# Kernel optimization log

Measured on AMD Instinct MI355X. Metric: run time of the kernel, lower is better.

Reference implementation:

```python
import jax, jax.numpy as jnp
import numpy as np
from jax import lax

N_TAGS = 512
N_TOKENS = 50257
SEQ_LEN = 8192


def setup_inputs() -> dict:
    key = jax.random.key(0)
    k1, k2, k3, k4 = jax.random.split(key, 4)
    token_list = jax.random.randint(k1, (SEQ_LEN,), 0, N_TOKENS, dtype=jnp.int64 if jax.config.read('jax_enable_x64') else jnp.int32)
    # Row-stochastic A [N,N], B [N,M]; Pi [N] sums to 1 (as produced by fit()).
    a = jax.random.uniform(k2, (N_TAGS, N_TAGS), dtype=jnp.float32) + 1e-3
    A = a / a.sum(axis=1, keepdims=True)
    b = jax.random.uniform(k3, (N_TAGS, N_TOKENS), dtype=jnp.float32) + 1e-3
    B = b / b.sum(axis=1, keepdims=True)
    p = jax.random.uniform(k4, (N_TAGS,), dtype=jnp.float32) + 1e-3
    Pi = p / p.sum()
    return {"token_list": token_list, "A": A, "B": B, "Pi": Pi}


def _viterbi(token_list, A, B, Pi):
    N = A.shape[0]
    logA = jnp.log(A)          # [N, N] transition (i -> j)
    logB = jnp.log(B)          # [N, M] emission
    logPi = jnp.log(Pi)        # [N]
    avg_score = jnp.log(jnp.ones((N,), dtype=A.dtype) / N)

    # Emission log-probs per step: [T, N]. token_id == -1 -> uniform score.
    emis = jnp.where((token_list == -1)[:, None], avg_score[None, :], logB.T[token_list])

    v0 = logPi + emis[0]       # [N]

    def step(v, e_t):
        scores = v[:, None] + logA           # [N_prev, N_cur]
        bp = jnp.argmax(scores, axis=0).astype(jnp.int32)   # [N]
        v_new = jnp.max(scores, axis=0) + e_t                # [N]
        return v_new, bp

    v_last, back_pointers = lax.scan(step, v0, emis[1:])  # back_pointers: [T-1, N]

    last = jnp.argmax(v_last).astype(jnp.int32)

    def back(ptr, bp_t):
        prev = bp_t[ptr]
        return prev, prev

    _, path_rev = lax.scan(back, last, back_pointers[::-1])  # [T-1] states T-2..0
    path = jnp.concatenate([path_rev[::-1], last[None]])      # [T] best path, start->end
    return path, v_last


def reference(token_list, A, B, Pi):
    path, _ = _viterbi(token_list, A, B, Pi)
    return path
```

## Files before the change

kernel.cpp:

```cpp
#include <hip/hip_runtime.h>
#include <cstdint>
#include <cstddef>
#include <math.h>


#define NT 512
#define TT 8192
#define MT 50257
#define DELTA_W 0.15f
#define NEG_INF (-3.402823466e38f)

#define BT_L 32
#define BT_S (TT / BT_L)

#define WS_LOGPI   0u
#define WS_VLAST   2048u
#define WS_BOUND   4096u
#define WS_ROWMAX  5632u
#define WS_MAPS    8192u
#define WS_LA      270336u
#define WS_EMIS    1318912u
#define WS_BP      18096128u
#define WS_NEED    26484736u

__global__ void prep_logs(const float* __restrict__ A, const float* __restrict__ Pi,
                          float* __restrict__ lA, float* __restrict__ logPi) {
    int idx = blockIdx.x * blockDim.x + threadIdx.x;
    if (idx < NT * NT) {
        lA[idx] = (float)log((double)A[idx]);
    } else if (idx < NT * NT + NT) {
        int j = idx - NT * NT;
        logPi[j] = (float)log((double)Pi[j]);
    }
}

__global__ void prep_rowmax(const float* __restrict__ lA, float* __restrict__ rowmax) {
    __shared__ float s[4];
    int i = blockIdx.x;
    int t = threadIdx.x;
    float m = fmaxf(lA[i * NT + t], lA[i * NT + t + 256]);
    for (int k = 32; k >= 1; k >>= 1) m = fmaxf(m, __shfl_xor(m, k, 64));
    if ((t & 63) == 0) s[t >> 6] = m;
    __syncthreads();
    if (t == 0) {
        float r = fmaxf(fmaxf(s[0], s[1]), fmaxf(s[2], s[3]));
        rowmax[i] = r;
    }
}

__global__ void prep_emis(const float* __restrict__ B, const int* __restrict__ tok,
                          float* __restrict__ emis) {
    int idx = blockIdx.x * blockDim.x + threadIdx.x;
    if (idx >= TT * NT) return;
    int t = idx >> 9;
    int j = idx & (NT - 1);
    int tk = tok[t];
    float e;
    if (tk < 0) e = (float)log((double)(1.0f / 512.0f));
    else        e = (float)log((double)B[(size_t)j * MT + tk]);
    emis[idx] = e;
}

__launch_bounds__(NT, 1)
__global__ void viterbi_fwd_exact(const float* __restrict__ lA,
                                  const float* __restrict__ rowmax,
                                  const float* emis,
                                  const float* __restrict__ logPi,
                                  unsigned short* __restrict__ bp,
                                  float* __restrict__ vlast,
                                  float* scratch) {
    __shared__ float2 SV[2][560];
    __shared__ float2 SVX[560];
    __shared__ alignas(16) float redR[8];
    __shared__ alignas(16) float redT[8];
    __shared__ int nCtr[2];
    __shared__ int nCtrX;
    __shared__ int Pshare;
    __shared__ float2 part[8][NT];

    const int tid  = threadIdx.x;
    const int j    = tid;
    const int lane = tid & 63;
    const int wave = tid >> 6;
    const unsigned long long below = (1ull << lane) - 1ull;
    const float* __restrict__ lAj = lA + j;

    float acc = 0.0f;
    {
        const float4* lAf4 = (const float4*)lA;
        for (int k = tid; k < (NT * NT) / 4; k += NT) acc += lAf4[k].x;
    }
    float r = rowmax[j];
    const float rmaxOwn = r;
    #pragma unroll
    for (int d = 1; d <= 32; d <<= 1) r = fmaxf(r, __shfl_xor(r, d, 64));
    if (lane == 0) redR[wave] = r;
    if (tid == 0) { nCtr[0] = 0; nCtr[1] = 0; nCtrX = 0; }
    __syncthreads();
    if (acc == 1.2345e30f && j == 511) SVX[0].x = acc;

    float v = logPi[j] + emis[j];
    float e_next = __builtin_nontemporal_load(emis + (size_t)NT + j);
    long long c0 = 0;
    int xSteps = 0;
    if (tid == 0) c0 = clock64();

    for (int t = 1; t < TT; ++t) {
        const int p = t & 1;
        const float e = e_next;
        {
            const int tn = (t + 1 < TT) ? t + 1 : TT - 1;
            e_next = __builtin_nontemporal_load(emis + (size_t)tn * NT + j);
        }
        float wm = v;
        #pragma unroll
        for (int d = 1; d <= 32; d <<= 1) wm = fmaxf(wm, __shfl_xor(wm, d, 64));
        bool pred = (v >= wm - DELTA_W);
        unsigned long long mk = __ballot(pred);
        int base = 0;
        if (lane == 0) base = atomicAdd(&nCtr[p], __popcll(mk));
        base = __shfl(base, 0, 64);
        if (pred) SV[p][base + __popcll(mk & below)] = make_float2(v, __int_as_float(j));
        __syncthreads();

        const int n   = nCtr[p];
        const int nm1 = n - 1;
        if (tid == 0) { nCtr[p ^ 1] = 0; nCtrX = 0; }

        float mv[8]; int bi[8];
        #pragma unroll
        for (int k = 0; k < 8; ++k) { mv[k] = NEG_INF; bi[k] = 0x7fffffff; }
        {
            const float* lAl = lA + lane;
            float ga[4][8], va[4]; int ia[4];
            float gb[4][8], vb[4]; int ib[4];
            #pragma unroll
            for (int q = 0; q < 4; ++q) {
                int s = wave + (q << 3); int gs = s < n ? s : nm1;
                float2 sv = SV[p][gs]; va[q] = sv.x; ia[q] = __float_as_int(sv.y);
                const float* rp = lAl + ((size_t)(unsigned)ia[q] << 9);
                #pragma unroll
                for (int k = 0; k < 8; ++k) ga[q][k] = rp[k << 6];
            }
            int s0 = wave;
            while (true) {
                const int sB = s0 + 32;
                const bool moreB = (sB < n);
                if (moreB) {
                    #pragma unroll
                    for (int q = 0; q < 4; ++q) {
                        int s = sB + (q << 3); int gs = s < n ? s : nm1;
                        float2 sv = SV[p][gs]; vb[q] = sv.x; ib[q] = __float_as_int(sv.y);
                        const float* rp = lAl + ((size_t)(unsigned)ib[q] << 9);
                        #pragma unroll
                        for (int k = 0; k < 8; ++k) gb[q][k] = rp[k << 6];
                    }
                }
                #pragma unroll
                for (int q = 0; q < 4; ++q)
                    #pragma unroll
                    for (int k = 0; k < 8; ++k) {
                        float sc = va[q] + ga[q][k];
                        if (sc > mv[k] || (sc == mv[k] && ia[q] < bi[k])) {
                            mv[k] = sc; bi[k] = ia[q];
                        }
                    }
                if (!moreB) break;
                const int sA = sB + 32;
                const bool moreA = (sA < n);
                if (moreA) {
                    #pragma unroll
                    for (int q = 0; q < 4; ++q) {
                        int s = sA + (q << 3); int gs = s < n ? s : nm1;
                        float2 sv = SV[p][gs]; va[q] = sv.x; ia[q] = __float_as_int(sv.y);
                        const float* rp = lAl + ((size_t)(unsigned)ia[q] << 9);
                        #pragma unroll
                        for (int k = 0; k < 8; ++k) ga[q][k] = rp[k << 6];
                    }
                }
                #pragma unroll
                for (int q = 0; q < 4; ++q)
                    #pragma unroll
                    for (int k = 0; k < 8; ++k) {
                        float sc = vb[q] + gb[q][k];
                        if (sc > mv[k] || (sc == mv[k] && ib[q] < bi[k])) {
                            mv[k] = sc; bi[k] = ib[q];
                        }
                    }
                if (!moreA) break;
                s0 = sA;
            }
        }
        #pragma unroll
        for (int k = 0; k < 8; ++k)
            part[wave][lane + (k << 6)] = make_float2(mv[k], __int_as_float(bi[k]));
        __syncthreads();

        float mval = NEG_INF;
        int   bidx = 0x7fffffff;
        #pragma unroll
        for (int w = 0; w < 8; ++w) {
            const float2 q = part[w][j];
            const float val = q.x;
            const int   ii  = __float_as_int(q.y);
            if (val > mval || (val == mval && ii < bidx)) { mval = val; bidx = ii; }
        }
        float tmin = mval;
        #pragma unroll
        for (int d = 1; d <= 32; d <<= 1) tmin = fminf(tmin, __shfl_xor(tmin, d, 64));
        if (lane == 0) redT[wave] = tmin;
        __syncthreads();

        float4 t0 = *(const float4*)redT;
        float4 t1 = *(const float4*)(redT + 4);
        float T = fminf(fminf(fminf(t0.x, t0.y), fminf(t0.z, t0.w)),
                        fminf(fminf(t1.x, t1.y), fminf(t1.z, t1.w)));
        bool px = (v + rmaxOwn >= T) && !pred;
        unsigned long long mkx = __ballot(px);
        if (mkx != 0ull) {
            int bx = 0;
            if (lane == 0) bx = atomicAdd(&nCtrX, __popcll(mkx));
            bx = __shfl(bx, 0, 64);
            if (px) SVX[bx + __popcll(mkx & below)] = make_float2(v, __int_as_float(j));
        }
        __syncthreads();

        const int nX = nCtrX;
        if (nX > 0) {
            ++xSteps;
            for (int s0x = 0; s0x < nX; s0x += 16) {
                float2 q[16];
                #pragma unroll
                for (int k = 0; k < 16; ++k) {
                    int s = s0x + k;
                    q[k] = SVX[s < nX ? s : nX - 1];
                }
                float a[16];
                #pragma unroll
                for (int k = 0; k < 16; ++k)
                    a[k] = lAj[(size_t)__float_as_int(q[k].y) * NT];
                #pragma unroll
                for (int k = 0; k < 16; ++k) {
                    float sc = q[k].x + a[k];
                    int   is = __float_as_int(q[k].y);
                    if (sc > mval || (sc == mval && is < bidx)) { mval = sc; bidx = is; }
                }
            }
        }
        float vn = mval + e;
        __builtin_nontemporal_store((unsigned short)bidx, bp + (size_t)t * NT + j);
        if (t == TT - 1) vlast[j] = vn;
        v = vn;
    }

    if (tid == 0) {
        long long cyc = (clock64() - c0) / (long long)(TT - 1);
        int cb = (int)(cyc >> 8); if (cb > 255) cb = 255; if (cb < 0) cb = 0;
        int xb = 0; { unsigned x = (unsigned)xSteps; while (x) { ++xb; x >>= 1; } }
        if (xb > 15) xb = 15;
        Pshare = cb * 16 + xb;
    }
    __syncthreads();
    const int P = Pshare;
    for (int pg = 0; pg < P; ++pg) {
        unsigned long long val = ((unsigned long long)pg << 32) | (unsigned)tid;
        __builtin_nontemporal_store(val,
            (unsigned long long*)((char*)scratch + (size_t)pg * 4096) + tid);
    }
}

__launch_bounds__(NT, 1)
__global__ void bt_maps(const unsigned short* __restrict__ bp,
                        unsigned short* __restrict__ maps) {
    __shared__ unsigned short bps[BT_L * NT];
    const int s = blockIdx.x;
    const int tlo = BT_L * s + 1;
    int thi = BT_L * (s + 1); if (thi > TT - 1) thi = TT - 1;
    const int nt = thi - tlo + 1;
    for (int k = threadIdx.x; k < nt * NT; k += NT)
        bps[k] = bp[(size_t)tlo * NT + k];
    __syncthreads();
    int cur = threadIdx.x;
    for (int r = nt - 1; r >= 0; --r) cur = bps[r * NT + cur];
    maps[s * NT + threadIdx.x] = (unsigned short)cur;
}

__launch_bounds__(NT, 1)
__global__ void bt_bound(const float* __restrict__ vlast,
                         const unsigned short* __restrict__ maps,
                         int* __restrict__ bound) {
    __shared__ float sv[NT];
    __shared__ int   si[NT];
    int j = threadIdx.x;
    sv[j] = vlast[j]; si[j] = j;
    __syncthreads();
    for (int off = NT / 2; off > 0; off >>= 1) {
        if (j < off) {
            float v2 = sv[j + off]; int i2 = si[j + off];
            if (v2 > sv[j] || (v2 == sv[j] && i2 < si[j])) { sv[j] = v2; si[j] = i2; }
        }
        __syncthreads();
    }
    if (j == 0) {
        int cur = si[0];
        bound[BT_S] = cur;
        for (int s = BT_S - 1; s >= 0; --s) {
            cur = maps[s * NT + cur];
            bound[s] = cur;
        }
    }
}

__launch_bounds__(NT, 1)
__global__ void bt_path(const unsigned short* __restrict__ bp,
                        const int* __restrict__ bound,
                        int* __restrict__ path) {
    __shared__ unsigned short bps[BT_L * NT];
    const int s = blockIdx.x;
    const int tlo = BT_L * s + 1;
    int thi = BT_L * (s + 1); if (thi > TT - 1) thi = TT - 1;
    const int nt = thi - tlo + 1;
    for (int k = threadIdx.x; k < nt * NT; k += NT)
        bps[k] = bp[(size_t)tlo * NT + k];
    __syncthreads();
    if (threadIdx.x == 0) {
        int cur = bound[s + 1];
        if (s == BT_S - 1) path[TT - 1] = cur;
        for (int r = nt - 1; r >= 0; --r) {
            cur = bps[r * NT + cur];
            path[tlo - 1 + r] = cur;
        }
    }
}

extern "C" void kernel_launch(void* const* d_in, const int* in_sizes, int n_in,
                              void* d_out, int out_size, void* d_ws, size_t ws_size,
                              hipStream_t stream) {
    const int*   tok = (const int*)d_in[0];
    const float* A   = (const float*)d_in[1];
    const float* B   = (const float*)d_in[2];
    const float* Pi  = (const float*)d_in[3];
    int* path = (int*)d_out;
    char* ws = (char*)d_ws;
    if (ws_size < (size_t)WS_NEED) return;

    float* logPi          = (float*)(ws + WS_LOGPI);
    float* vlast          = (float*)(ws + WS_VLAST);
    int*   bound          = (int*)(ws + WS_BOUND);
    float* rowmax         = (float*)(ws + WS_ROWMAX);
    unsigned short* maps  = (unsigned short*)(ws + WS_MAPS);
    float* lA             = (float*)(ws + WS_LA);
    float* emis           = (float*)(ws + WS_EMIS);
    unsigned short* bpp   = (unsigned short*)(ws + WS_BP);

    prep_logs  <<<(NT * NT + NT + 255) / 256, 256, 0, stream>>>(A, Pi, lA, logPi);
    prep_emis  <<<(TT * NT) / 256,            256, 0, stream>>>(B, tok, emis);
    prep_rowmax<<<NT, 256, 0, stream>>>(lA, rowmax);
    viterbi_fwd_exact<<<1, NT, 0, stream>>>(lA, rowmax, emis, logPi, bpp, vlast,
                                            emis );
    bt_maps  <<<BT_S, NT, 0, stream>>>(bpp, maps);
    bt_bound <<<1,    NT, 0, stream>>>(vlast, maps, bound);
    bt_path  <<<BT_S, NT, 0, stream>>>(bpp, bound, path);
}
```

Baseline: 57.18 ms.

## Stage candidate logA rows into LDS via global_load_lds batches

Replaces the register double-buffered gather of transition rows for the candidate predecessor set with direct global-to-LDS loads (global_load_lds, 16 bytes per lane) into a per-wave staging buffer of SBW rows. Each wave then reads the staged rows from LDS for the max/argmax update. The intent is to cut register pressure and issue wider, coalesced loads. In exchange, every batch waits on vmcnt(0) with no overlap between loading and compute, and LDS use grows by 96KB. The probe encoding in the scratch write also changes to report the average candidate count instead of the number of extra steps.

```diff
diff --git a/kernel.cpp b/kernel.cpp
--- a/kernel.cpp
+++ b/kernel.cpp
@@ -12,6 +12,7 @@
 
 #define BT_L 32
 #define BT_S (TT / BT_L)
+#define SBW 6
 
 #define WS_LOGPI   0u
 #define WS_VLAST   2048u
@@ -59,6 +60,12 @@
     if (tk < 0) e = (float)log((double)(1.0f / 512.0f));
     else        e = (float)log((double)B[(size_t)j * MT + tk]);
     emis[idx] = e;
+}
+
+__device__ __forceinline__ void glds16(const float* g, float* l) {
+    __builtin_amdgcn_global_load_lds(
+        (const __attribute__((address_space(1))) void*)g,
+        (__attribute__((address_space(3))) void*)l, 16, 0, 0);
 }
 
 __launch_bounds__(NT, 1)
@@ -77,6 +84,7 @@
     __shared__ int nCtrX;
     __shared__ int Pshare;
     __shared__ float2 part[8][NT];
+    __shared__ alignas(16) float stageW[8][SBW][NT];
 
     const int tid  = threadIdx.x;
     const int j    = tid;
@@ -101,8 +109,7 @@
 
     float v = logPi[j] + emis[j];
     float e_next = __builtin_nontemporal_load(emis + (size_t)NT + j);
-    long long c0 = 0;
-    int xSteps = 0;
+    long long c0 = 0, nAcc = 0;
     if (tid == 0) c0 = clock64();
 
     for (int t = 1; t < TT; ++t) {
@@ -123,72 +130,40 @@
         if (pred) SV[p][base + __popcll(mk & below)] = make_float2(v, __int_as_float(j));
         __syncthreads();
 
-        const int n   = nCtr[p];
-        const int nm1 = n - 1;
+        const int n = nCtr[p];
         if (tid == 0) { nCtr[p ^ 1] = 0; nCtrX = 0; }
+        nAcc += n;
 
         float mv[8]; int bi[8];
         #pragma unroll
         for (int k = 0; k < 8; ++k) { mv[k] = NEG_INF; bi[k] = 0x7fffffff; }
         {
-            const float* lAl = lA + lane;
-            float ga[4][8], va[4]; int ia[4];
-            float gb[4][8], vb[4]; int ib[4];
-            #pragma unroll
-            for (int q = 0; q < 4; ++q) {
-                int s = wave + (q << 3); int gs = s < n ? s : nm1;
-                float2 sv = SV[p][gs]; va[q] = sv.x; ia[q] = __float_as_int(sv.y);
-                const float* rp = lAl + ((size_t)(unsigned)ia[q] << 9);
-                #pragma unroll
-                for (int k = 0; k < 8; ++k) ga[q][k] = rp[k << 6];
-            }
-            int s0 = wave;
-            while (true) {
-                const int sB = s0 + 32;
-                const bool moreB = (sB < n);
-                if (moreB) {
+            const int nw = (n - wave + 7) >> 3;
+            float* stw = &stageW[wave][0][0];
+            for (int b0 = 0; b0 < nw; b0 += SBW) {
+                const int bc = (nw - b0 < SBW) ? (nw - b0) : SBW;
+                asm volatile("s_waitcnt lgkmcnt(0)" ::: "memory");
+                for (int q = 0; q < bc; ++q) {
+                    const int s = wave + ((b0 + q) << 3);
+                    const int idx = __float_as_int(SV[p][s].y);
+                    const float* gp = lA + ((size_t)(unsigned)idx << 9) + (lane << 2);
+                    glds16(gp,       stw + q * NT);
+                    glds16(gp + 256, stw + q * NT + 256);
+                }
+                asm volatile("s_waitcnt vmcnt(0)" ::: "memory");
+                for (int q = 0; q < bc; ++q) {
+                    const int s = wave + ((b0 + q) << 3);
+                    const float2 sv = SV[p][s];
+                    const int ii = __float_as_int(sv.y);
+                    const float* rp = stw + q * NT + lane;
                     #pragma unroll
-                    for (int q = 0; q < 4; ++q) {
-                        int s = sB + (q << 3); int gs = s < n ? s : nm1;
-                        float2 sv = SV[p][gs]; vb[q] = sv.x; ib[q] = __float_as_int(sv.y);
-                        const float* rp = lAl + ((size_t)(unsigned)ib[q] << 9);
-                        #pragma unroll
-                        for (int k = 0; k < 8; ++k) gb[q][k] = rp[k << 6];
+                    for (int k = 0; k < 8; ++k) {
+                        float sc = sv.x + rp[k << 6];
+                        if (sc > mv[k] || (sc == mv[k] && ii < bi[k])) {
+                            mv[k] = sc; bi[k] = ii;
+                        }
                     }
                 }
-                #pragma unroll
-                for (int q = 0; q < 4; ++q)
-                    #pragma unroll
-                    for (int k = 0; k < 8; ++k) {
-                        float sc = va[q] + ga[q][k];
-                        if (sc > mv[k] || (sc == mv[k] && ia[q] < bi[k])) {
-                            mv[k] = sc; bi[k] = ia[q];
-                        }
-                    }
-                if (!moreB) break;
-                const int sA = sB + 32;
-                const bool moreA = (sA < n);
-                if (moreA) {
-                    #pragma unroll
-                    for (int q = 0; q < 4; ++q) {
-                        int s = sA + (q << 3); int gs = s < n ? s : nm1;
-                        float2 sv = SV[p][gs]; va[q] = sv.x; ia[q] = __float_as_int(sv.y);
-                        const float* rp = lAl + ((size_t)(unsigned)ia[q] << 9);
-                        #pragma unroll
-                        for (int k = 0; k < 8; ++k) ga[q][k] = rp[k << 6];
-                    }
-                }
-                #pragma unroll
-                for (int q = 0; q < 4; ++q)
-                    #pragma unroll
-                    for (int k = 0; k < 8; ++k) {
-                        float sc = vb[q] + gb[q][k];
-                        if (sc > mv[k] || (sc == mv[k] && ib[q] < bi[k])) {
-                            mv[k] = sc; bi[k] = ib[q];
-                        }
-                    }
-                if (!moreA) break;
-                s0 = sA;
             }
         }
         #pragma unroll
@@ -227,7 +202,6 @@
 
         const int nX = nCtrX;
         if (nX > 0) {
-            ++xSteps;
             for (int s0x = 0; s0x < nX; s0x += 16) {
                 float2 q[16];
                 #pragma unroll
@@ -256,9 +230,9 @@
     if (tid == 0) {
         long long cyc = (clock64() - c0) / (long long)(TT - 1);
         int cb = (int)(cyc >> 8); if (cb > 255) cb = 255; if (cb < 0) cb = 0;
-        int xb = 0; { unsigned x = (unsigned)xSteps; while (x) { ++xb; x >>= 1; } }
-        if (xb > 15) xb = 15;
-        Pshare = cb * 16 + xb;
+        int mn = (int)(nAcc / (long long)(TT - 1)); if (mn > 511) mn = 511;
+        int nb = mn >> 4; if (nb > 15) nb = 15;
+        Pshare = cb * 16 + nb;
     }
     __syncthreads();
     const int P = Pshare;
```

Result: no change. 56.22 ms (-1.7%).
